# Performance work log

Measured on AMD Instinct MI355X. Metric: run time of the kernel, lower is better.

The kernel has to match this reference:

```python
import jax, jax.numpy as jnp
import numpy as np

EPS = 1e-8

def _normalize(a):
    return a / jnp.clip(jnp.linalg.norm(a, axis=-1, keepdims=True), EPS)

def _cosine(a, b):
    # pairwise cosine similarity: [Na, d] x [Nb, d] -> [Na, Nb]
    return _normalize(a) @ _normalize(b).T

def setup_inputs() -> dict:
    key = jax.random.key(0)
    n, k, q, d = 100, 5, 75, 4096
    x = jax.random.normal(key, (n * (k + q), d), dtype=jnp.float32)
    tao = jnp.full((1,), 10.0, dtype=jnp.float32)
    return {"x": x, "tao": tao, "n": n, "k": k, "q": q}

def reference(x, tao, n, k, q):
    d = x.shape[-1]
    x = x.reshape(n, k + q, d)
    support = x[:, :k]                      # [n, k, d]
    query = x[:, k:].reshape(n * q, d)      # [NQ, d]
    NQ = n * q
    proto = support.mean(axis=1)            # [n, d]

    pre_sim = _cosine(query, proto)         # [NQ, n]
    pre_label = jnp.argmax(pre_sim, axis=1) # [NQ]

    # vectorized per-class masked softmax aggregation (replaces Python loop)
    cls_ids = jnp.arange(n)
    mask = pre_label[None, :] == cls_ids[:, None]            # [n, NQ]
    logits_q = jnp.where(mask, pre_sim.T, -jnp.inf)          # [n, NQ]
    proto_n = _normalize(proto)
    self_sim = jnp.sum(proto_n * proto_n, axis=-1)           # [n], cosine(proto, proto)
    logits = jnp.concatenate([logits_q, self_sim[:, None]], axis=1)  # [n, NQ+1]
    w = jax.nn.softmax(logits, axis=1)                       # [n, NQ+1]
    adapted_proto = w[:, :NQ] @ query + w[:, NQ:] * proto    # [n, d]

    sim = _cosine(query, adapted_proto)                      # [NQ, n]
    return tao.reshape(()) * sim
```

## Files before the change

### kernel.cpp

```cpp
#include <hip/hip_runtime.h>
#include <hip/hip_bf16.h>
#include <math.h>

#define NQUERY 7500
#define NCLS   100
#define DIM    4096
#define KQ     75
#define KSUP   5
#define RPC    80
#define MPAD   7552
#define NPAD   112
#define CAPQ   256
#define RCAP   2048
#define EPSF   1e-8f

typedef __attribute__((ext_vector_type(8))) short bf16x8;
typedef __attribute__((ext_vector_type(4))) short s16x4;
typedef __attribute__((ext_vector_type(4))) float f32x4;

__device__ __forceinline__ int xrow_of_query(int j) {
    return (j / KQ) * RPC + KSUP + (j % KQ);
}
__device__ __forceinline__ short bf16t(float x) {
    union { float f; unsigned u; } v; v.f = x;
    return (short)(v.u >> 16);
}
__device__ __forceinline__ void gload_lds16(const short* g, short* l) {
    __builtin_amdgcn_global_load_lds(
        (const __attribute__((address_space(1))) unsigned int*)g,
        (__attribute__((address_space(3))) unsigned int*)l, 16, 0, 0);
}
__device__ __forceinline__ size_t tile_off(int nt, int lm, int i) {
    return (((size_t)(nt * 128 + (i >> 5)) * 4 + ((i >> 3) & 3)) * 16 + lm) * 8 + (i & 7);
}

__global__ __launch_bounds__(256) void k_proto(const float* __restrict__ x,
        float* __restrict__ proto, short* __restrict__ Phi, float* __restrict__ es,
        double* __restrict__ pninv) {
    const int c = blockIdx.x, t = threadIdx.x;
    const int nt = c >> 4, lm = c & 15;
    if (c >= NCLS) {
        for (int g = t; g < 512; g += 256) {
            const int kstep = g >> 2, kq = g & 3;
            size_t o = (((size_t)(nt * 128 + kstep) * 4 + kq) * 16 + lm) * 8;
            bf16x8 z = {0,0,0,0,0,0,0,0};
            *(bf16x8*)(Phi + o) = z;
        }
        if (t == 0) es[c] = 0.f;
        return;
    }
    __shared__ double red[4];
    __shared__ float s_inv;
    const float* b0 = x + (size_t)(c * RPC) * DIM;
    float v[16];
    double ssq = 0.0;
#pragma unroll
    for (int p = 0; p < 4; ++p) {
        const int i = p * 1024 + t * 4;
        f32x4 s = {0.f, 0.f, 0.f, 0.f};
#pragma unroll
        for (int r = 0; r < KSUP; ++r)
            s += *(const f32x4*)(b0 + (size_t)r * DIM + i);
        s = s / 5.0f;
        *(f32x4*)&v[p*4] = s;
        *(f32x4*)(proto + (size_t)c*DIM + i) = s;
        ssq += (double)s[0]*s[0] + (double)s[1]*s[1]
             + (double)s[2]*s[2] + (double)s[3]*s[3];
    }
    for (int o = 32; o; o >>= 1) ssq += __shfl_down(ssq, o);
    if ((t & 63) == 0) red[t >> 6] = ssq;
    __syncthreads();
    if (t == 0) {
        double dtot = red[0] + red[1] + red[2] + red[3];
        pninv[c] = 1.0 / sqrt(dtot);
        float tot = (float)dtot;
        float inv = 1.f / fmaxf(sqrtf(tot), EPSF);
        s_inv = inv;
        es[c] = expf(tot * inv * inv);
    }
    __syncthreads();
    const float inv = s_inv;
#pragma unroll
    for (int p = 0; p < 4; ++p) {
        const int i = p * 1024 + t * 4;
        s16x4 h;
#pragma unroll
        for (int e = 0; e < 4; ++e) h[e] = bf16t(v[p*4+e] * inv);
        *(s16x4*)(Phi + tile_off(nt, lm, i)) = h;
    }
}

template<bool SSQ>
__global__ __launch_bounds__(256) void k_gemm(const float* __restrict__ x,
        const short* __restrict__ Bt, float* __restrict__ Sd, float* __restrict__ nq2) {
    __shared__ short sbuf[7 * 8 * 512];
    const int g = blockIdx.x, kz = blockIdx.y;
    const int w = threadIdx.x >> 6, lane = threadIdx.x & 63;
    const int lm = lane & 15, kq = lane >> 4;
    const int ks0 = kz * 8;

#pragma unroll
    for (int p = 0; p < 14; ++p) {
        const int idx = w * 14 + p;
        const short* gsrc = Bt + (((size_t)((idx >> 3) * 128 + ks0 + (idx & 7))) << 9) + lane * 8;
        gload_lds16(gsrc, sbuf + ((size_t)idx << 9));
    }

    const int mt0 = g + 32 * w;
    const int mt1 = g + 32 * (w + 4);
    const int mt2 = g + 32 * (w + 8);
    const int mt3 = g + 32 * (w + 12);
    const bool v0 = mt0 < 472, v1 = mt1 < 472, v2 = mt2 < 472, v3 = mt3 < 472;

    auto apt = [&](int mt) {
        const int j = mt * 16 + lm;
        const int jc = j < NQUERY ? j : NQUERY - 1;
        return x + (size_t)xrow_of_query(jc) * DIM + kz * 256 + kq * 8;
    };

    f32x4 A0[16], A1[16];
#define LOADA(buf, mt) do { \
        const float* pa_ = apt(mt); \
        _Pragma("unroll") \
        for (int s_ = 0; s_ < 8; ++s_) { \
            buf[s_*2]   = *(const f32x4*)(pa_ + s_*32); \
            buf[s_*2+1] = *(const f32x4*)(pa_ + s_*32 + 4); \
        } } while (0)

    if (v0) LOADA(A0, mt0);
    if (v1) LOADA(A1, mt1);
    __syncthreads();

#define COMPUTE(buf, mt) do { \
        f32x4 acc_[7]; \
        _Pragma("unroll") \
        for (int nt_ = 0; nt_ < 7; ++nt_) acc_[nt_] = (f32x4){0.f,0.f,0.f,0.f}; \
        float ssq_ = 0.f; \
        _Pragma("unroll") \
        for (int s_ = 0; s_ < 8; ++s_) { \
            float f_[8] = {buf[s_*2][0],buf[s_*2][1],buf[s_*2][2],buf[s_*2][3], \
                           buf[s_*2+1][0],buf[s_*2+1][1],buf[s_*2+1][2],buf[s_*2+1][3]}; \
            bf16x8 ah_; \
            _Pragma("unroll") \
            for (int e_ = 0; e_ < 8; ++e_) { \
                if (SSQ) ssq_ += f_[e_] * f_[e_]; \
                ah_[e_] = bf16t(f_[e_]); \
            } \
            _Pragma("unroll") \
            for (int nt_ = 0; nt_ < 7; ++nt_) { \
                const bf16x8 bh_ = *(const bf16x8*)(sbuf + (((size_t)(nt_*8 + s_)) << 9) + lane*8); \
                acc_[nt_] = __builtin_amdgcn_mfma_f32_16x16x32_bf16(ah_, bh_, acc_[nt_], 0, 0, 0); \
            } \
        } \
        if (SSQ) { \
            ssq_ += __shfl_xor(ssq_, 16); ssq_ += __shfl_xor(ssq_, 32); \
            const int j_ = (mt) * 16 + lm; \
            if (kq == 0 && j_ < NQUERY) atomicAdd(&nq2[j_], ssq_); \
        } \
        float* sp_ = Sd + (size_t)((mt) * 16) * NPAD; \
        _Pragma("unroll") \
        for (int nt_ = 0; nt_ < 7; ++nt_) \
            _Pragma("unroll") \
            for (int r_ = 0; r_ < 4; ++r_) \
                atomicAdd(&sp_[(size_t)(kq * 4 + r_) * NPAD + nt_ * 16 + lm], acc_[nt_][r_]); \
    } while (0)

    if (v0) COMPUTE(A0, mt0);
    if (v2) LOADA(A0, mt2);
    if (v1) COMPUTE(A1, mt1);
    if (v3) LOADA(A1, mt3);
    if (v2) COMPUTE(A0, mt2);
    if (v3) COMPUTE(A1, mt3);
#undef LOADA
#undef COMPUTE
}

__global__ __launch_bounds__(256) void k_argmax(const float* __restrict__ S,
        const float* __restrict__ nq2, float* __restrict__ coef, float* __restrict__ invq,
        int* __restrict__ pos, int* __restrict__ ccnt, int* __restrict__ cls_list,
        int* __restrict__ rcnt, int* __restrict__ rlist) {
    const int j = blockIdx.x * 256 + threadIdx.x;
    if (j >= NQUERY) return;
    const float* row = S + (size_t)j * NPAD;
    float m1 = -1e30f, m2 = -1e30f;
    int i1 = 0, i2 = 0;
    for (int c = 0; c < NCLS; ++c) {
        float v = row[c];
        if (v > m1) { m2 = m1; i2 = i1; m1 = v; i1 = c; }
        else if (v > m2) { m2 = v; i2 = c; }
    }
    const float inv = 1.f / fmaxf(sqrtf(nq2[j]), EPSF);
    invq[j] = inv;
    coef[j] = expf(m1 * inv);
    const int p = atomicAdd(&ccnt[i1], 1);
    if (p < CAPQ) { cls_list[i1 * CAPQ + p] = j; pos[j] = p; }
    else pos[j] = -1;
    if ((m1 - m2) * inv < 5e-4f) {
        int rp = atomicAdd(rcnt, 1);
        if (rp < RCAP) rlist[rp] = j | (i1 << 13) | (i2 << 20);
    }
}

__global__ __launch_bounds__(256) void k_refine(const float* __restrict__ x,
        const float* __restrict__ proto, const double* __restrict__ pninv,
        const float* __restrict__ S, const float* __restrict__ invq,
        float* __restrict__ coef, const int* __restrict__ pos,
        int* __restrict__ ccnt, int* __restrict__ cls_list,
        const int* __restrict__ rcnt, const int* __restrict__ rlist) {
    const int cnt = min(*rcnt, RCAP);
    const int t = threadIdx.x;
    __shared__ double red1[4], red2[4];
    for (int e = blockIdx.x; e < cnt; e += gridDim.x) {
        const int pk = rlist[e];
        const int j = pk & 8191, c1 = (pk >> 13) & 127, c2 = (pk >> 20) & 127;
        const float* xq = x + (size_t)xrow_of_query(j) * DIM;
        const float* p1 = proto + (size_t)c1 * DIM;
        const float* p2 = proto + (size_t)c2 * DIM;
        double d1 = 0.0, d2 = 0.0;
        for (int i = t; i < DIM; i += 256) {
            const double qv = (double)xq[i];
            d1 += (double)p1[i] * qv;
            d2 += (double)p2[i] * qv;
        }
        for (int o = 32; o; o >>= 1) { d1 += __shfl_down(d1, o); d2 += __shfl_down(d2, o); }
        if ((t & 63) == 0) { red1[t >> 6] = d1; red2[t >> 6] = d2; }
        __syncthreads();
        if (t == 0) {
            const double cos1 = (red1[0]+red1[1]+red1[2]+red1[3]) * pninv[c1];
            const double cos2 = (red2[0]+red2[1]+red2[2]+red2[3]) * pninv[c2];
            const int win = (cos2 > cos1 || (cos2 == cos1 && c2 < c1)) ? c2 : c1;
            if (win != c1) {
                coef[j] = expf(S[(size_t)j * NPAD + win] * invq[j]);
                const int pj = pos[j];
                if (pj >= 0) cls_list[c1 * CAPQ + pj] = -1;
                const int np = atomicAdd(&ccnt[c2], 1);
                if (np < CAPQ) cls_list[c2 * CAPQ + np] = j;
            }
        }
        __syncthreads();
    }
}

__global__ __launch_bounds__(128) void k_adapt(const float* __restrict__ x,
        const float* __restrict__ coef, const int* __restrict__ cls_cnt,
        const int* __restrict__ cls_list, float* __restrict__ APpart) {
    __shared__ int   s_j[CAPQ];
    __shared__ float s_cf[CAPQ];
    const int cx = blockIdx.x, c = blockIdx.y, sl = blockIdx.z;
    const int n = min(cls_cnt[c], CAPQ);
    for (int e = threadIdx.x; e < n; e += 128) {
        const int j = cls_list[c * CAPQ + e];
        s_j[e] = j;
        s_cf[e] = (j >= 0) ? coef[j] : 0.f;
    }
    __syncthreads();
    const int i0 = cx * 512 + threadIdx.x * 4;
    f32x4 acc = {0.f, 0.f, 0.f, 0.f};
    for (int e = sl; e < n; e += 4) {
        const int j = s_j[e];
        if (j >= 0) {
            const float cf = s_cf[e];
            const f32x4 v = *(const f32x4*)(x + (size_t)xrow_of_query(j) * DIM + i0);
            acc += v * cf;
        }
    }
    *(f32x4*)(APpart + (size_t)sl * NCLS * DIM + (size_t)c * DIM + i0) = acc;
}

__global__ __launch_bounds__(256) void k_apnorm(const float* __restrict__ APpart,
        const float* __restrict__ proto, const float* __restrict__ es,
        short* __restrict__ APhi) {
    const int c = blockIdx.x, t = threadIdx.x;
    const int nt = c >> 4, lm = c & 15;
    if (c >= NCLS) {
        for (int g = t; g < 512; g += 256) {
            const int kstep = g >> 2, kq = g & 3;
            size_t o = (((size_t)(nt * 128 + kstep) * 4 + kq) * 16 + lm) * 8;
            bf16x8 z = {0,0,0,0,0,0,0,0};
            *(bf16x8*)(APhi + o) = z;
        }
        return;
    }
    __shared__ float red[4];
    __shared__ float s_inv;
    const float e0 = es[c];
    float v[16];
    float ssq = 0.f;
#pragma unroll
    for (int p = 0; p < 4; ++p) {
        const int i = p * 1024 + t * 4;
        f32x4 s = {0.f, 0.f, 0.f, 0.f};
#pragma unroll
        for (int sl = 0; sl < 4; ++sl)
            s += *(const f32x4*)(APpart + (size_t)sl * NCLS * DIM + (size_t)c * DIM + i);
        f32x4 pr = *(const f32x4*)(proto + (size_t)c*DIM + i);
        s += pr * e0;
        *(f32x4*)&v[p*4] = s;
        ssq += s[0]*s[0] + s[1]*s[1] + s[2]*s[2] + s[3]*s[3];
    }
    for (int o = 32; o; o >>= 1) ssq += __shfl_down(ssq, o);
    if ((t & 63) == 0) red[t >> 6] = ssq;
    __syncthreads();
    if (t == 0) {
        float tot = red[0] + red[1] + red[2] + red[3];
        s_inv = 1.f / fmaxf(sqrtf(tot), EPSF);
    }
    __syncthreads();
    const float inv = s_inv;
#pragma unroll
    for (int p = 0; p < 4; ++p) {
        const int i = p * 1024 + t * 4;
        s16x4 h;
#pragma unroll
        for (int e = 0; e < 4; ++e) h[e] = bf16t(v[p*4+e] * inv);
        *(s16x4*)(APhi + tile_off(nt, lm, i)) = h;
    }
}

__global__ __launch_bounds__(256) void k_scale(const float* __restrict__ Ored,
        const float* __restrict__ invq, const float* __restrict__ tao,
        float* __restrict__ out) {
    const int idx = blockIdx.x * 256 + threadIdx.x;
    if (idx >= NQUERY * 25) return;
    const int j = idx / 25, c4 = (idx % 25) * 4;
    const f32x4 s = *(const f32x4*)(Ored + (size_t)j * NPAD + c4);
    const float sc = tao[0] * invq[j];
    *(f32x4*)(out + (size_t)j * NCLS + c4) = s * sc;
}

#define OFF_RCNT   0u
#define OFF_CCNT   256u
#define OFF_NQ2    1792u
#define ZERO_BYTES 32768u
#define OFF_ES     32768u
#define OFF_INVQ   33280u
#define OFF_POS    63488u
#define OFF_COEF   93696u
#define OFF_RLIST  123904u
#define OFF_CLIST  132096u
#define OFF_PNINV  234496u
#define OFF_PROTO  235520u
#define OFF_PHI    1873920u
#define OFF_APHI   2791424u
#define OFF_SRED   3708928u
#define OFF_ORED   7092224u
#define OFF_APPART 10475520u

extern "C" void kernel_launch(void* const* d_in, const int* in_sizes, int n_in,
                              void* d_out, int out_size, void* d_ws, size_t ws_size,
                              hipStream_t stream) {
    const float* x   = (const float*)d_in[0];
    const float* tao = (const float*)d_in[1];
    char* ws = (char*)d_ws;

    int*    rcnt   = (int*)   (ws + OFF_RCNT);
    int*    ccnt   = (int*)   (ws + OFF_CCNT);
    float*  nq2    = (float*) (ws + OFF_NQ2);
    float*  es     = (float*) (ws + OFF_ES);
    float*  invq   = (float*) (ws + OFF_INVQ);
    int*    pos    = (int*)   (ws + OFF_POS);
    float*  coef   = (float*) (ws + OFF_COEF);
    int*    rlist  = (int*)   (ws + OFF_RLIST);
    int*    clist  = (int*)   (ws + OFF_CLIST);
    double* pninv  = (double*)(ws + OFF_PNINV);
    float*  proto  = (float*) (ws + OFF_PROTO);
    short*  Phi    = (short*) (ws + OFF_PHI);
    short*  APhi   = (short*) (ws + OFF_APHI);
    float*  Sred   = (float*) (ws + OFF_SRED);
    float*  Ored   = (float*) (ws + OFF_ORED);
    float*  APpart = (float*) (ws + OFF_APPART);

    hipMemsetAsync(ws, 0, ZERO_BYTES, stream);
    hipMemsetAsync(ws + OFF_SRED, 0, 2u * 3383296u, stream);

    k_proto <<<NPAD, 256, 0, stream>>>(x, proto, Phi, es, pninv);
    k_gemm<true> <<<dim3(32, 16), 256, 0, stream>>>(x, Phi, Sred, nq2);
    k_argmax <<<30, 256, 0, stream>>>(Sred, nq2, coef, invq, pos, ccnt, clist, rcnt, rlist);
    k_refine <<<512, 256, 0, stream>>>(x, proto, pninv, Sred, invq, coef, pos, ccnt, clist, rcnt, rlist);
    k_adapt  <<<dim3(8, NCLS, 4), 128, 0, stream>>>(x, coef, ccnt, clist, APpart);
    k_apnorm <<<NPAD, 256, 0, stream>>>(APpart, proto, es, APhi);
    k_gemm<false><<<dim3(32, 16), 256, 0, stream>>>(x, APhi, Ored, nq2);
    k_scale  <<<733, 256, 0, stream>>>(Ored, invq, tao, (float*)d_out);
}
```

Baseline: 339.3 us.

## Restructure GEMM split-K into 4-way partials with double-buffered LDS staging

The bf16 MFMA GEMM changes from a 16-way K split that atomically accumulated into a zeroed output to a 4-way split. Each wave now owns one M tile and walks 1024 K elements, double-buffering B tiles in LDS and A rows in registers. Partial results are written with plain stores to separate buffers and summed in a new reduce kernel, or inside the scale kernel for the second GEMM. This removes the large memset and the float atomics in exchange for an extra reduction pass, more partial-buffer traffic, and more barriers per block.

```diff
diff --git a/kernel.cpp b/kernel.cpp
--- a/kernel.cpp
+++ b/kernel.cpp
@@ -13,6 +13,7 @@
 #define CAPQ   256
 #define RCAP   2048
 #define EPSF   1e-8f
+#define SELEM  845824
 
 typedef __attribute__((ext_vector_type(8))) short bf16x8;
 typedef __attribute__((ext_vector_type(4))) short s16x4;
@@ -92,87 +93,93 @@
 
 template<bool SSQ>
 __global__ __launch_bounds__(256) void k_gemm(const float* __restrict__ x,
-        const short* __restrict__ Bt, float* __restrict__ Sd, float* __restrict__ nq2) {
-    __shared__ short sbuf[7 * 8 * 512];
-    const int g = blockIdx.x, kz = blockIdx.y;
+        const short* __restrict__ Bt, float* __restrict__ Part, float* __restrict__ nq2) {
+    __shared__ short sbuf[2][28 * 512];
+    const int bx = blockIdx.x, kz = blockIdx.y;
     const int w = threadIdx.x >> 6, lane = threadIdx.x & 63;
     const int lm = lane & 15, kq = lane >> 4;
-    const int ks0 = kz * 8;
-
-#pragma unroll
-    for (int p = 0; p < 14; ++p) {
-        const int idx = w * 14 + p;
-        const short* gsrc = Bt + (((size_t)((idx >> 3) * 128 + ks0 + (idx & 7))) << 9) + lane * 8;
-        gload_lds16(gsrc, sbuf + ((size_t)idx << 9));
-    }
-
-    const int mt0 = g + 32 * w;
-    const int mt1 = g + 32 * (w + 4);
-    const int mt2 = g + 32 * (w + 8);
-    const int mt3 = g + 32 * (w + 12);
-    const bool v0 = mt0 < 472, v1 = mt1 < 472, v2 = mt2 < 472, v3 = mt3 < 472;
-
-    auto apt = [&](int mt) {
-        const int j = mt * 16 + lm;
-        const int jc = j < NQUERY ? j : NQUERY - 1;
-        return x + (size_t)xrow_of_query(jc) * DIM + kz * 256 + kq * 8;
-    };
-
-    f32x4 A0[16], A1[16];
-#define LOADA(buf, mt) do { \
-        const float* pa_ = apt(mt); \
+    const int mt = bx * 4 + w;
+    const int j = mt * 16 + lm;
+    const int jc = j < NQUERY ? j : NQUERY - 1;
+    const float* pa = x + (size_t)xrow_of_query(jc) * DIM + kq * 8;
+    const int ks0 = kz * 32;
+
+    f32x4 acc[7];
+#pragma unroll
+    for (int nt = 0; nt < 7; ++nt) acc[nt] = (f32x4){0.f,0.f,0.f,0.f};
+    float ssq = 0.f;
+    f32x4 Ar0[8], Ar1[8];
+
+#define STAGE(c_, b_) do { \
         _Pragma("unroll") \
-        for (int s_ = 0; s_ < 8; ++s_) { \
-            buf[s_*2]   = *(const f32x4*)(pa_ + s_*32); \
-            buf[s_*2+1] = *(const f32x4*)(pa_ + s_*32 + 4); \
+        for (int p_ = 0; p_ < 7; ++p_) { \
+            const int idx_ = w * 7 + p_;                \
+            const int nt_ = idx_ >> 2, s_ = idx_ & 3; \
+            const short* gsrc_ = Bt + (((size_t)(nt_ * 128 + ks0 + (c_) * 4 + s_)) << 9) + lane * 8; \
+            gload_lds16(gsrc_, &sbuf[b_][idx_ << 9]); \
         } } while (0)
 
-    if (v0) LOADA(A0, mt0);
-    if (v1) LOADA(A1, mt1);
-    __syncthreads();
-
-#define COMPUTE(buf, mt) do { \
-        f32x4 acc_[7]; \
+#define LOADA(c_, buf_) do { \
         _Pragma("unroll") \
-        for (int nt_ = 0; nt_ < 7; ++nt_) acc_[nt_] = (f32x4){0.f,0.f,0.f,0.f}; \
-        float ssq_ = 0.f; \
+        for (int s_ = 0; s_ < 4; ++s_) { \
+            buf_[s_*2]   = *(const f32x4*)(pa + (size_t)(ks0 + (c_)*4 + s_) * 32); \
+            buf_[s_*2+1] = *(const f32x4*)(pa + (size_t)(ks0 + (c_)*4 + s_) * 32 + 4); \
+        } } while (0)
+
+#define COMPUTE(b_, buf_) do { \
         _Pragma("unroll") \
-        for (int s_ = 0; s_ < 8; ++s_) { \
-            float f_[8] = {buf[s_*2][0],buf[s_*2][1],buf[s_*2][2],buf[s_*2][3], \
-                           buf[s_*2+1][0],buf[s_*2+1][1],buf[s_*2+1][2],buf[s_*2+1][3]}; \
+        for (int s_ = 0; s_ < 4; ++s_) { \
+            float fv_[8] = {buf_[s_*2][0],buf_[s_*2][1],buf_[s_*2][2],buf_[s_*2][3], \
+                            buf_[s_*2+1][0],buf_[s_*2+1][1],buf_[s_*2+1][2],buf_[s_*2+1][3]}; \
             bf16x8 ah_; \
             _Pragma("unroll") \
             for (int e_ = 0; e_ < 8; ++e_) { \
-                if (SSQ) ssq_ += f_[e_] * f_[e_]; \
-                ah_[e_] = bf16t(f_[e_]); \
+                if (SSQ) ssq += fv_[e_] * fv_[e_]; \
+                ah_[e_] = bf16t(fv_[e_]); \
             } \
             _Pragma("unroll") \
             for (int nt_ = 0; nt_ < 7; ++nt_) { \
-                const bf16x8 bh_ = *(const bf16x8*)(sbuf + (((size_t)(nt_*8 + s_)) << 9) + lane*8); \
-                acc_[nt_] = __builtin_amdgcn_mfma_f32_16x16x32_bf16(ah_, bh_, acc_[nt_], 0, 0, 0); \
+                const bf16x8 bh_ = *(const bf16x8*)(&sbuf[b_][((nt_*4 + s_) << 9) + lane*8]); \
+                acc[nt_] = __builtin_amdgcn_mfma_f32_16x16x32_bf16(ah_, bh_, acc[nt_], 0, 0, 0); \
             } \
-        } \
-        if (SSQ) { \
-            ssq_ += __shfl_xor(ssq_, 16); ssq_ += __shfl_xor(ssq_, 32); \
-            const int j_ = (mt) * 16 + lm; \
-            if (kq == 0 && j_ < NQUERY) atomicAdd(&nq2[j_], ssq_); \
-        } \
-        float* sp_ = Sd + (size_t)((mt) * 16) * NPAD; \
-        _Pragma("unroll") \
-        for (int nt_ = 0; nt_ < 7; ++nt_) \
-            _Pragma("unroll") \
-            for (int r_ = 0; r_ < 4; ++r_) \
-                atomicAdd(&sp_[(size_t)(kq * 4 + r_) * NPAD + nt_ * 16 + lm], acc_[nt_][r_]); \
-    } while (0)
-
-    if (v0) COMPUTE(A0, mt0);
-    if (v2) LOADA(A0, mt2);
-    if (v1) COMPUTE(A1, mt1);
-    if (v3) LOADA(A1, mt3);
-    if (v2) COMPUTE(A0, mt2);
-    if (v3) COMPUTE(A1, mt3);
+        } } while (0)
+
+    STAGE(0, 0); LOADA(0, Ar0);
+    __syncthreads();
+    STAGE(1, 1); LOADA(1, Ar1); COMPUTE(0, Ar0); __syncthreads();
+    STAGE(2, 0); LOADA(2, Ar0); COMPUTE(1, Ar1); __syncthreads();
+    STAGE(3, 1); LOADA(3, Ar1); COMPUTE(0, Ar0); __syncthreads();
+    STAGE(4, 0); LOADA(4, Ar0); COMPUTE(1, Ar1); __syncthreads();
+    STAGE(5, 1); LOADA(5, Ar1); COMPUTE(0, Ar0); __syncthreads();
+    STAGE(6, 0); LOADA(6, Ar0); COMPUTE(1, Ar1); __syncthreads();
+    STAGE(7, 1); LOADA(7, Ar1); COMPUTE(0, Ar0); __syncthreads();
+    COMPUTE(1, Ar1);
+#undef STAGE
 #undef LOADA
 #undef COMPUTE
+
+    if (SSQ) {
+        ssq += __shfl_xor(ssq, 16);
+        ssq += __shfl_xor(ssq, 32);
+        if (kq == 0 && j < NQUERY) atomicAdd(&nq2[j], ssq);
+    }
+    float* sp = Part + (size_t)kz * SELEM + (size_t)(mt * 16) * NPAD;
+#pragma unroll
+    for (int nt = 0; nt < 7; ++nt)
+#pragma unroll
+        for (int r = 0; r < 4; ++r)
+            sp[(size_t)(kq * 4 + r) * NPAD + nt * 16 + lm] = acc[nt][r];
+}
+
+__global__ __launch_bounds__(256) void k_reduce1(const float* __restrict__ Spart,
+        float* __restrict__ Sred) {
+    const int idx = blockIdx.x * 256 + threadIdx.x;
+    const size_t e = (size_t)idx * 4;
+    f32x4 s = {0.f, 0.f, 0.f, 0.f};
+#pragma unroll
+    for (int kz = 0; kz < 4; ++kz)
+        s += *(const f32x4*)(Spart + (size_t)kz * SELEM + e);
+    *(f32x4*)(Sred + e) = s;
 }
 
 __global__ __launch_bounds__(256) void k_argmax(const float* __restrict__ S,
@@ -317,13 +324,17 @@
     }
 }
 
-__global__ __launch_bounds__(256) void k_scale(const float* __restrict__ Ored,
+__global__ __launch_bounds__(256) void k_scale(const float* __restrict__ Opart,
         const float* __restrict__ invq, const float* __restrict__ tao,
         float* __restrict__ out) {
     const int idx = blockIdx.x * 256 + threadIdx.x;
     if (idx >= NQUERY * 25) return;
     const int j = idx / 25, c4 = (idx % 25) * 4;
-    const f32x4 s = *(const f32x4*)(Ored + (size_t)j * NPAD + c4);
+    const size_t e = (size_t)j * NPAD + c4;
+    f32x4 s = {0.f, 0.f, 0.f, 0.f};
+#pragma unroll
+    for (int kz = 0; kz < 4; ++kz)
+        s += *(const f32x4*)(Opart + (size_t)kz * SELEM + e);
     const float sc = tao[0] * invq[j];
     *(f32x4*)(out + (size_t)j * NCLS + c4) = s * sc;
 }
@@ -343,8 +354,8 @@
 #define OFF_PHI    1873920u
 #define OFF_APHI   2791424u
 #define OFF_SRED   3708928u
-#define OFF_ORED   7092224u
 #define OFF_APPART 10475520u
+#define OFF_PART   17029120u
 
 extern "C" void kernel_launch(void* const* d_in, const int* in_sizes, int n_in,
                               void* d_out, int out_size, void* d_ws, size_t ws_size,
@@ -367,18 +378,18 @@
     short*  Phi    = (short*) (ws + OFF_PHI);
     short*  APhi   = (short*) (ws + OFF_APHI);
     float*  Sred   = (float*) (ws + OFF_SRED);
-    float*  Ored   = (float*) (ws + OFF_ORED);
     float*  APpart = (float*) (ws + OFF_APPART);
+    float*  Part   = (float*) (ws + OFF_PART);
 
     hipMemsetAsync(ws, 0, ZERO_BYTES, stream);
-    hipMemsetAsync(ws + OFF_SRED, 0, 2u * 3383296u, stream);
 
     k_proto <<<NPAD, 256, 0, stream>>>(x, proto, Phi, es, pninv);
-    k_gemm<true> <<<dim3(32, 16), 256, 0, stream>>>(x, Phi, Sred, nq2);
+    k_gemm<true> <<<dim3(118, 4), 256, 0, stream>>>(x, Phi, Part, nq2);
+    k_reduce1<<<826, 256, 0, stream>>>(Part, Sred);
     k_argmax <<<30, 256, 0, stream>>>(Sred, nq2, coef, invq, pos, ccnt, clist, rcnt, rlist);
     k_refine <<<512, 256, 0, stream>>>(x, proto, pninv, Sred, invq, coef, pos, ccnt, clist, rcnt, rlist);
     k_adapt  <<<dim3(8, NCLS, 4), 128, 0, stream>>>(x, coef, ccnt, clist, APpart);
     k_apnorm <<<NPAD, 256, 0, stream>>>(APpart, proto, es, APhi);
-    k_gemm<false><<<dim3(32, 16), 256, 0, stream>>>(x, APhi, Ored, nq2);
-    k_scale  <<<733, 256, 0, stream>>>(Ored, invq, tao, (float*)d_out);
-}
+    k_gemm<false><<<dim3(118, 4), 256, 0, stream>>>(x, APhi, Part, nq2);
+    k_scale  <<<733, 256, 0, stream>>>(Part, invq, tao, (float*)d_out);
+}
```

Measured after the change: 302.7 us. 10.8% less time.
